# Optimization experiments

Hardware: AMD Instinct MI355X
Metric: run time of the kernel (lower is better)

## Reference

```python
import jax, jax.numpy as jnp
import numpy as np

DIM = 64  # per-head dim; temperature init = sqrt(DIM)
B, H, S, D = 4, 12, 2048, 64


def setup_inputs() -> dict:
    key = jax.random.key(0)
    kq, kk, kv = jax.random.split(key, 3)
    Q = jax.random.normal(kq, (B, H, S, D), dtype=jnp.float32)
    K = jax.random.normal(kk, (B, H, S, D), dtype=jnp.float32)
    V = jax.random.normal(kv, (B, H, S, D), dtype=jnp.float32)
    temperature = jnp.ones((1,), dtype=jnp.float32) * (DIM ** 0.5)
    return {"Q": Q, "K": K, "V": V, "temperature": temperature}


def reference(Q, K, V, temperature):
    # scores: [B,H,S,S]
    scores = jnp.einsum("bhqd,bhkd->bhqk", Q, K) / temperature
    s = scores.shape[-1]
    eye = jnp.eye(s, dtype=bool)  # diagonal self-exclusion
    scores = jnp.where(eye, -jnp.inf, scores)
    attn = jax.nn.softmax(scores, axis=-1)
    return jnp.einsum("bhqk,bhkd->bhqd", attn, V)
```

## Files before the change

### kernel.cpp

```cpp
#include <hip/hip_runtime.h>
#include <hip/hip_bf16.h>

#define S_LEN 2048
#define D_DIM 64
#define NHEADS 48
#define QT 128
#define KT 64
#define NKT (S_LEN / KT)
#define HEAD_ELEMS ((size_t)S_LEN * D_DIM)
#define WS_NEED (3ull * NHEADS * S_LEN * D_DIM * 2ull)

typedef short bf16x8 __attribute__((ext_vector_type(8)));
typedef float f32x4 __attribute__((ext_vector_type(4)));

__device__ __forceinline__ unsigned short f2bf(float x) {
    unsigned u = __builtin_bit_cast(unsigned, x);
    u = (u + 0x7fffu + ((u >> 16) & 1u)) >> 16;
    return (unsigned short)u;
}

__device__ __forceinline__ unsigned cvtpk(float lo, float hi) {
    unsigned r;
    asm("v_cvt_pk_bf16_f32 %0, %1, %2" : "=v"(r) : "v"(lo), "v"(hi));
    return r;
}

__global__ __launch_bounds__(256) void lsa_prep(
    const float* __restrict__ Qg, const float* __restrict__ Kg,
    const float* __restrict__ Vg, const float* __restrict__ Tg,
    unsigned short* __restrict__ Qs, unsigned short* __restrict__ Kf,
    unsigned short* __restrict__ Vf) {
    const int b   = blockIdx.x;
    const int tid = threadIdx.x;
    const int r   = tid >> 4;
    const int c4  = (tid & 15) * 4;

    __shared__ __align__(16) unsigned short Kl[4096];
    __shared__ __align__(16) unsigned short Vl[4096];

    const size_t ibase = (size_t)b * 4096;
    const float qscale = 1.442695041f / Tg[0];

#pragma unroll
    for (int it = 0; it < 4; ++it) {
        const int rr = it * 16 + r;
        const size_t off = ibase + (size_t)rr * D_DIM + c4;

        float4 q4 = *(const float4*)(Qg + off);
        uint2 qo;
        qo.x = cvtpk(q4.x * qscale, q4.y * qscale);
        qo.y = cvtpk(q4.z * qscale, q4.w * qscale);
        *(uint2*)&Qs[off] = qo;

        float4 k4 = *(const float4*)(Kg + off);
        {
            const int f = rr >> 4, l15 = rr & 15;
            const int c = c4 >> 5, lhi = (c4 >> 3) & 3, j0 = c4 & 7;
            uint2 ko;
            ko.x = cvtpk(k4.x, k4.y);
            ko.y = cvtpk(k4.z, k4.w);
            *(uint2*)&Kl[c * 2048 + f * 512 + ((lhi << 4) | l15) * 8 + j0] = ko;
        }

        float4 v4 = *(const float4*)(Vg + off);
        {
            const int cc = rr >> 5, rem = rr & 31;
            const int jv = ((rem >> 4) << 2) | (rem & 3);
            const int lhiv = (rem >> 2) & 3;
            const int g = c4 >> 4;
            const int base = cc * 2048 + g * 512 + (lhiv << 7) + jv;
            Vl[base + ((c4 + 0) & 15) * 8] = f2bf(v4.x);
            Vl[base + ((c4 + 1) & 15) * 8] = f2bf(v4.y);
            Vl[base + ((c4 + 2) & 15) * 8] = f2bf(v4.z);
            Vl[base + ((c4 + 3) & 15) * 8] = f2bf(v4.w);
        }
    }
    __syncthreads();
    const uint4* ks = (const uint4*)Kl;
    const uint4* vs = (const uint4*)Vl;
    uint4* kd = (uint4*)(Kf + ibase);
    uint4* vd = (uint4*)(Vf + ibase);
    kd[tid]       = ks[tid];
    kd[tid + 256] = ks[tid + 256];
    vd[tid]       = vs[tid];
    vd[tid + 256] = vs[tid + 256];
}

__global__ __launch_bounds__(256, 2) void lsa_attn_pipe(
    const unsigned short* __restrict__ Qs, const unsigned short* __restrict__ Kf,
    const unsigned short* __restrict__ Vf, float* __restrict__ Og) {

    const int bid  = blockIdx.x;
    const int xcd  = bid & 7;
    const int idx  = bid >> 3;
    const int bh   = xcd * 6 + (idx >> 4);
    const int qt   = idx & 15;
    const int tid  = threadIdx.x;
    const int wid  = tid >> 6;
    const int lane = tid & 63;
    const int l15  = lane & 15;
    const int lhi  = lane >> 4;

    const unsigned short* Qh = Qs + (size_t)bh * HEAD_ELEMS;
    const char* Kh = (const char*)(Kf + (size_t)bh * HEAD_ELEMS) + lane * 16;
    const char* Vh = (const char*)(Vf + (size_t)bh * HEAD_ELEMS) + lane * 16;
    float* Ob = Og + (size_t)bh * HEAD_ELEMS;

    const int qbase   = qt * QT + wid * 32;
    const int diag_kt = qbase >> 6;

    bf16x8 qf[2][2];
#pragma unroll
    for (int rb = 0; rb < 2; ++rb) {
#pragma unroll
        for (int c = 0; c < 2; ++c) {
            qf[rb][c] = *(const bf16x8*)(Qh + (size_t)(qbase + rb * 16 + l15) * D_DIM
                                            + c * 32 + lhi * 8);
        }
    }

    const f32x4 zero4 = {0.f, 0.f, 0.f, 0.f};
    f32x4 acc[2][4];
    float mrow[2], lp[2];
#pragma unroll
    for (int rb = 0; rb < 2; ++rb) {
#pragma unroll
        for (int g = 0; g < 4; ++g) acc[rb][g] = zero4;
        mrow[rb] = -1e30f; lp[rb] = 0.f;
    }

    bf16x8 kr[8], vr[8];
    f32x4 sf[2][4];
    bf16x8 pb[2][2];

#define LOADK(T) do {                                                          \
    const char* p_ = Kh + (size_t)(T) * 8192;                                  \
    _Pragma("unroll")                                                          \
    for (int u = 0; u < 8; ++u) {                                              \
        kr[u] = *(const bf16x8*)(p_ + (u >> 2) * 4096 + (u & 3) * 1024);       \
    }                                                                          \
} while (0)

#define LOADV(T) do {                                                          \
    const char* p_ = Vh + (size_t)(T) * 8192;                                  \
    _Pragma("unroll")                                                          \
    for (int u = 0; u < 8; ++u) {                                              \
        vr[u] = *(const bf16x8*)(p_ + (u >> 2) * 4096 + (u & 3) * 1024);       \
    }                                                                          \
} while (0)

#define QK() do {                                                              \
    _Pragma("unroll")                                                          \
    for (int rb = 0; rb < 2; ++rb) {                                           \
        _Pragma("unroll")                                                      \
        for (int f = 0; f < 4; ++f) sf[rb][f] = zero4;                         \
    }                                                                          \
    __builtin_amdgcn_s_setprio(1);                                             \
    _Pragma("unroll")                                                          \
    for (int c = 0; c < 2; ++c) {                                              \
        _Pragma("unroll")                                                      \
        for (int rb = 0; rb < 2; ++rb) {                                       \
            _Pragma("unroll")                                                  \
            for (int f = 0; f < 4; ++f) {                                      \
                sf[rb][f] = __builtin_amdgcn_mfma_f32_16x16x32_bf16(           \
                    kr[c * 4 + f], qf[rb][c], sf[rb][f], 0, 0, 0);             \
            }                                                                  \
        }                                                                      \
    }                                                                          \
    __builtin_amdgcn_s_setprio(0);                                             \
} while (0)

#define PV() do {                                                              \
    __builtin_amdgcn_s_setprio(1);                                             \
    _Pragma("unroll")                                                          \
    for (int cc = 0; cc < 2; ++cc) {                                           \
        _Pragma("unroll")                                                      \
        for (int rb = 0; rb < 2; ++rb) {                                       \
            _Pragma("unroll")                                                  \
            for (int g = 0; g < 4; ++g) {                                      \
                acc[rb][g] = __builtin_amdgcn_mfma_f32_16x16x32_bf16(          \
                    vr[cc * 4 + g], pb[rb][cc], acc[rb][g], 0, 0, 0);          \
            }                                                                  \
        }                                                                      \
    }                                                                          \
    __builtin_amdgcn_s_setprio(0);                                             \
} while (0)

#define SM(T) do {                                                             \
    if ((T) == diag_kt) {                                                      \
        const int kb0_ = (T) * KT;                                             \
        _Pragma("unroll")                                                      \
        for (int rb = 0; rb < 2; ++rb) {                                       \
            const int q_ = qbase + rb * 16 + l15;                              \
            _Pragma("unroll")                                                  \
            for (int f = 0; f < 4; ++f) {                                      \
                _Pragma("unroll")                                              \
                for (int i = 0; i < 4; ++i) {                                  \
                    const int k_ = kb0_ + f * 16 + lhi * 4 + i;                \
                    if (q_ == k_) sf[rb][f][i] = -1e30f;                       \
                }                                                              \
            }                                                                  \
        }                                                                      \
    }                                                                          \
    _Pragma("unroll")                                                          \
    for (int rb = 0; rb < 2; ++rb) {                                           \
        f32x4 mv_;                                                             \
        _Pragma("unroll")                                                      \
        for (int i = 0; i < 4; ++i) {                                          \
            mv_[i] = fmaxf(fmaxf(sf[rb][0][i], sf[rb][1][i]),                  \
                           fmaxf(sf[rb][2][i], sf[rb][3][i]));                 \
        }                                                                      \
        const float pm_ = fmaxf(fmaxf(mv_[0], mv_[1]), fmaxf(mv_[2], mv_[3]));  \
        if (__any(pm_ > mrow[rb] + 8.0f)) {                                    \
            float m0_ = pm_;                                                   \
            m0_ = fmaxf(m0_, __shfl_xor(m0_, 16));                             \
            m0_ = fmaxf(m0_, __shfl_xor(m0_, 32));                             \
            const float mnew_ = fmaxf(mrow[rb], m0_);                          \
            const float al_ = __builtin_amdgcn_exp2f(mrow[rb] - mnew_);        \
            mrow[rb] = mnew_;                                                  \
            lp[rb] *= al_;                                                     \
            _Pragma("unroll")                                                  \
            for (int g = 0; g < 4; ++g) acc[rb][g] *= al_;                     \
        }                                                                      \
        f32x4 ps_ = zero4;                                                     \
        _Pragma("unroll")                                                      \
        for (int f = 0; f < 4; ++f) {                                          \
            _Pragma("unroll")                                                  \
            for (int i = 0; i < 4; ++i) {                                      \
                sf[rb][f][i] = __builtin_amdgcn_exp2f(sf[rb][f][i] - mrow[rb]); \
            }                                                                  \
            ps_ += sf[rb][f];                                                  \
        }                                                                      \
        lp[rb] += (ps_[0] + ps_[1]) + (ps_[2] + ps_[3]);                       \
        _Pragma("unroll")                                                      \
        for (int cc = 0; cc < 2; ++cc) {                                       \
            uint4 u_;                                                          \
            u_.x = cvtpk(sf[rb][cc * 2][0],     sf[rb][cc * 2][1]);            \
            u_.y = cvtpk(sf[rb][cc * 2][2],     sf[rb][cc * 2][3]);            \
            u_.z = cvtpk(sf[rb][cc * 2 + 1][0], sf[rb][cc * 2 + 1][1]);        \
            u_.w = cvtpk(sf[rb][cc * 2 + 1][2], sf[rb][cc * 2 + 1][3]);        \
            pb[rb][cc] = __builtin_bit_cast(bf16x8, u_);                       \
        }                                                                      \
    }                                                                          \
} while (0)

    LOADK(0);
    LOADV(0);
    QK();

#pragma unroll 1
    for (int t = 0; t < NKT - 1; ++t) {
        LOADK(t + 1);
        __builtin_amdgcn_sched_barrier(0);
        SM(t);
        QK();
        PV();
        LOADV(t + 1);
    }
    SM(NKT - 1);
    PV();

#undef LOADK
#undef LOADV
#undef QK
#undef PV
#undef SM

#pragma unroll
    for (int rb = 0; rb < 2; ++rb) {
        float l = lp[rb];
        l += __shfl_xor(l, 16);
        l += __shfl_xor(l, 32);
        const float invl = 1.0f / l;
        const int q = qbase + rb * 16 + l15;
#pragma unroll
        for (int g = 0; g < 4; ++g) {
            float4 o;
            o.x = acc[rb][g][0] * invl;
            o.y = acc[rb][g][1] * invl;
            o.z = acc[rb][g][2] * invl;
            o.w = acc[rb][g][3] * invl;
            *(float4*)(Ob + (size_t)q * D_DIM + g * 16 + lhi * 4) = o;
        }
    }
}

__device__ __forceinline__ int swzK_fb(int row, int col) {
    return (row << 6) + (col ^ ((row & 7) << 3));
}
__device__ __forceinline__ int swzV_fb(int row, int col) {
    int f = (row ^ (row >> 3)) & 7;
    return (row << 6) + (col ^ (f << 3));
}

__global__ __launch_bounds__(256, 2) void lsa_attn_fb(
    const float* __restrict__ Qg, const float* __restrict__ Kg,
    const float* __restrict__ Vg, const float* __restrict__ Tg,
    float* __restrict__ Og) {

    const int bid  = blockIdx.x;
    const int bh   = bid >> 4;
    const int qt   = bid & 15;
    const int tid  = threadIdx.x;
    const int wid  = tid >> 6;
    const int lane = tid & 63;
    const int l15  = lane & 15;
    const int lhi  = lane >> 4;

    __shared__ __align__(16) unsigned short Kt[KT * D_DIM];
    __shared__ __align__(16) unsigned short Vt[D_DIM * KT];

    const size_t base = (size_t)bh * HEAD_ELEMS;
    const float* Qb = Qg + base;
    const float* Kb = Kg + base;
    const float* Vb = Vg + base;
    float*       Ob = Og + base;

    const float inv_t = 1.0f / Tg[0];
    const int qbase = qt * QT + wid * 32;
    const int diag_kt = qbase >> 6;

    bf16x8 qf[2][2];
#pragma unroll
    for (int rb = 0; rb < 2; ++rb) {
#pragma unroll
        for (int c = 0; c < 2; ++c) {
            const float* src = Qb + (size_t)(qbase + rb * 16 + l15) * D_DIM + c * 32 + lhi * 8;
            float4 a = *(const float4*)(src);
            float4 b = *(const float4*)(src + 4);
            bf16x8 v;
            v[0] = (short)f2bf(a.x * inv_t); v[1] = (short)f2bf(a.y * inv_t);
            v[2] = (short)f2bf(a.z * inv_t); v[3] = (short)f2bf(a.w * inv_t);
            v[4] = (short)f2bf(b.x * inv_t); v[5] = (short)f2bf(b.y * inv_t);
            v[6] = (short)f2bf(b.z * inv_t); v[7] = (short)f2bf(b.w * inv_t);
            qf[rb][c] = v;
        }
    }

    const f32x4 zero4 = {0.f, 0.f, 0.f, 0.f};
    f32x4 acc[2][4];
    float mrow[2], lrow[2];
#pragma unroll
    for (int rb = 0; rb < 2; ++rb) {
#pragma unroll
        for (int g = 0; g < 4; ++g) acc[rb][g] = zero4;
        mrow[rb] = -1e30f; lrow[rb] = 0.f;
    }

    const int ld_r = tid >> 4;
    const int ld_c = (tid & 15) * 4;
    float4 kreg[4], vreg[4];

#define LOAD_TILE(KT_IDX) do {                                                 \
    const int kb0_ = (KT_IDX) * KT;                                            \
    _Pragma("unroll")                                                          \
    for (int it = 0; it < 4; ++it) {                                           \
        const int r_ = it * 16 + ld_r;                                         \
        kreg[it] = *(const float4*)(Kb + (size_t)(kb0_ + r_) * D_DIM + ld_c);  \
        vreg[it] = *(const float4*)(Vb + (size_t)(kb0_ + r_) * D_DIM + ld_c);  \
    }                                                                          \
} while (0)

    LOAD_TILE(0);

    for (int kt = 0; kt < NKT; ++kt) {
        const int kb0 = kt * KT;
        __syncthreads();
#pragma unroll
        for (int it = 0; it < 4; ++it) {
            const int r = it * 16 + ld_r;
            unsigned lo = (unsigned)f2bf(kreg[it].x) | ((unsigned)f2bf(kreg[it].y) << 16);
            unsigned hi = (unsigned)f2bf(kreg[it].z) | ((unsigned)f2bf(kreg[it].w) << 16);
            *(uint2*)&Kt[swzK_fb(r, ld_c)] = make_uint2(lo, hi);
            Vt[swzV_fb(ld_c + 0, r)] = f2bf(vreg[it].x);
            Vt[swzV_fb(ld_c + 1, r)] = f2bf(vreg[it].y);
            Vt[swzV_fb(ld_c + 2, r)] = f2bf(vreg[it].z);
            Vt[swzV_fb(ld_c + 3, r)] = f2bf(vreg[it].w);
        }
        __syncthreads();
        if (kt + 1 < NKT) LOAD_TILE(kt + 1);

        f32x4 sf[2][4];
#pragma unroll
        for (int rb = 0; rb < 2; ++rb) {
#pragma unroll
            for (int f = 0; f < 4; ++f) sf[rb][f] = zero4;
        }

#pragma unroll
        for (int c = 0; c < 2; ++c) {
            bf16x8 kb[4];
#pragma unroll
            for (int f = 0; f < 4; ++f)
                kb[f] = *(const bf16x8*)&Kt[swzK_fb(f * 16 + l15, c * 32 + lhi * 8)];
#pragma unroll
            for (int rb = 0; rb < 2; ++rb) {
#pragma unroll
                for (int f = 0; f < 4; ++f)
                    sf[rb][f] = __builtin_amdgcn_mfma_f32_16x16x32_bf16(
                        kb[f], qf[rb][c], sf[rb][f], 0, 0, 0);
            }
        }

        if (kt == diag_kt) {
#pragma unroll
            for (int rb = 0; rb < 2; ++rb) {
                const int q = qbase + rb * 16 + l15;
#pragma unroll
                for (int f = 0; f < 4; ++f) {
#pragma unroll
                    for (int i = 0; i < 4; ++i) {
                        const int k = kb0 + f * 16 + lhi * 4 + i;
                        if (q == k) sf[rb][f][i] = -1e30f;
                    }
                }
            }
        }

        bf16x8 pb[2][2];
#pragma unroll
        for (int rb = 0; rb < 2; ++rb) {
            f32x4 mv;
#pragma unroll
            for (int i = 0; i < 4; ++i)
                mv[i] = fmaxf(fmaxf(sf[rb][0][i], sf[rb][1][i]),
                              fmaxf(sf[rb][2][i], sf[rb][3][i]));
            float m0 = fmaxf(fmaxf(mv[0], mv[1]), fmaxf(mv[2], mv[3]));
            m0 = fmaxf(m0, __shfl_xor(m0, 16));
            m0 = fmaxf(m0, __shfl_xor(m0, 32));
            const float mnew  = fmaxf(mrow[rb], m0);
            const float alpha = __expf(mrow[rb] - mnew);
            mrow[rb] = mnew;
            f32x4 ps = zero4;
#pragma unroll
            for (int f = 0; f < 4; ++f) {
#pragma unroll
                for (int i = 0; i < 4; ++i)
                    sf[rb][f][i] = __expf(sf[rb][f][i] - mnew);
                ps += sf[rb][f];
            }
            float s0 = (ps[0] + ps[1]) + (ps[2] + ps[3]);
            s0 += __shfl_xor(s0, 16);
            s0 += __shfl_xor(s0, 32);
            lrow[rb] = lrow[rb] * alpha + s0;
#pragma unroll
            for (int g = 0; g < 4; ++g) acc[rb][g] *= alpha;
#pragma unroll
            for (int cc = 0; cc < 2; ++cc) {
                bf16x8 v;
#pragma unroll
                for (int j = 0; j < 8; ++j)
                    v[j] = (short)f2bf(sf[rb][cc * 2 + (j >> 2)][j & 3]);
                pb[rb][cc] = v;
            }
        }

#pragma unroll
        for (int cc = 0; cc < 2; ++cc) {
            bf16x8 va[4];
#pragma unroll
            for (int g = 0; g < 4; ++g) {
                const int row = g * 16 + l15;
                uint2 lo = *(const uint2*)&Vt[swzV_fb(row, cc * 32 + lhi * 4)];
                uint2 hi = *(const uint2*)&Vt[swzV_fb(row, cc * 32 + 16 + lhi * 4)];
                bf16x8 t;
                ((uint2*)&t)[0] = lo;
                ((uint2*)&t)[1] = hi;
                va[g] = t;
            }
#pragma unroll
            for (int rb = 0; rb < 2; ++rb) {
#pragma unroll
                for (int g = 0; g < 4; ++g)
                    acc[rb][g] = __builtin_amdgcn_mfma_f32_16x16x32_bf16(
                        va[g], pb[rb][cc], acc[rb][g], 0, 0, 0);
            }
        }
    }
#undef LOAD_TILE

#pragma unroll
    for (int rb = 0; rb < 2; ++rb) {
        const float invl = 1.0f / lrow[rb];
        const int q = qbase + rb * 16 + l15;
#pragma unroll
        for (int g = 0; g < 4; ++g) {
            float4 o;
            o.x = acc[rb][g][0] * invl;
            o.y = acc[rb][g][1] * invl;
            o.z = acc[rb][g][2] * invl;
            o.w = acc[rb][g][3] * invl;
            *(float4*)(Ob + (size_t)q * D_DIM + g * 16 + lhi * 4) = o;
        }
    }
}

extern "C" void kernel_launch(void* const* d_in, const int* in_sizes, int n_in,
                              void* d_out, int out_size, void* d_ws, size_t ws_size,
                              hipStream_t stream) {
    const float* Q = (const float*)d_in[0];
    const float* K = (const float*)d_in[1];
    const float* V = (const float*)d_in[2];
    const float* T = (const float*)d_in[3];
    float* O = (float*)d_out;

    if (ws_size >= WS_NEED) {
        unsigned short* Qs = (unsigned short*)d_ws;
        unsigned short* Kf = Qs + NHEADS * HEAD_ELEMS;
        unsigned short* Vf = Kf + NHEADS * HEAD_ELEMS;
        hipLaunchKernelGGL(lsa_prep, dim3(NHEADS * NKT), dim3(256), 0, stream,
                           Q, K, V, T, Qs, Kf, Vf);
        hipLaunchKernelGGL(lsa_attn_pipe, dim3(NHEADS * (S_LEN / QT)), dim3(256), 0, stream,
                           Qs, Kf, Vf, O);
    } else {
        hipLaunchKernelGGL(lsa_attn_fb, dim3(NHEADS * (S_LEN / QT)), dim3(256), 0, stream,
                           Q, K, V, T, O);
    }
}
```

Before: 88.41 us.

## Halve key tile and double-buffer score fragments in attention pipeline

```diff
diff --git a/kernel.cpp b/kernel.cpp
--- a/kernel.cpp
+++ b/kernel.cpp
@@ -5,7 +5,7 @@
 #define D_DIM 64
 #define NHEADS 48
 #define QT 128
-#define KT 64
+#define KT 32
 #define NKT (S_LEN / KT)
 #define HEAD_ELEMS ((size_t)S_LEN * D_DIM)
 #define WS_NEED (3ull * NHEADS * S_LEN * D_DIM * 2ull)
@@ -54,12 +54,13 @@
 
         float4 k4 = *(const float4*)(Kg + off);
         {
-            const int f = rr >> 4, l15 = rr & 15;
+            const int l15 = rr & 15;
             const int c = c4 >> 5, lhi = (c4 >> 3) & 3, j0 = c4 & 7;
             uint2 ko;
             ko.x = cvtpk(k4.x, k4.y);
             ko.y = cvtpk(k4.z, k4.w);
-            *(uint2*)&Kl[c * 2048 + f * 512 + ((lhi << 4) | l15) * 8 + j0] = ko;
+            *(uint2*)&Kl[(rr >> 5) * 2048 + c * 1024 + ((rr >> 4) & 1) * 512
+                         + ((lhi << 4) | l15) * 8 + j0] = ko;
         }
 
         float4 v4 = *(const float4*)(Vg + off);
@@ -86,7 +87,7 @@
     vd[tid + 256] = vs[tid + 256];
 }
 
-__global__ __launch_bounds__(256, 2) void lsa_attn_pipe(
+__global__ __launch_bounds__(256, 3) void lsa_attn_p2(
     const unsigned short* __restrict__ Qs, const unsigned short* __restrict__ Kf,
     const unsigned short* __restrict__ Vf, float* __restrict__ Og) {
 
@@ -107,7 +108,7 @@
     float* Ob = Og + (size_t)bh * HEAD_ELEMS;
 
     const int qbase   = qt * QT + wid * 32;
-    const int diag_kt = qbase >> 6;
+    const int diag_kt = qbase >> 5;
 
     bf16x8 qf[2][2];
 #pragma unroll
@@ -129,31 +130,30 @@
         mrow[rb] = -1e30f; lp[rb] = 0.f;
     }
 
-    bf16x8 kr[8], vr[8];
-    f32x4 sf[2][4];
-    bf16x8 pb[2][2];
+    bf16x8 kr[4], vr[4], pb[2];
+    f32x4 sfA[2][2], sfB[2][2];
 
 #define LOADK(T) do {                                                          \
-    const char* p_ = Kh + (size_t)(T) * 8192;                                  \
-    _Pragma("unroll")                                                          \
-    for (int u = 0; u < 8; ++u) {                                              \
-        kr[u] = *(const bf16x8*)(p_ + (u >> 2) * 4096 + (u & 3) * 1024);       \
+    const char* p_ = Kh + (size_t)(T) * 4096;                                  \
+    _Pragma("unroll")                                                          \
+    for (int u = 0; u < 4; ++u) {                                              \
+        kr[u] = *(const bf16x8*)(p_ + (u >> 1) * 2048 + (u & 1) * 1024);       \
     }                                                                          \
 } while (0)
 
 #define LOADV(T) do {                                                          \
-    const char* p_ = Vh + (size_t)(T) * 8192;                                  \
-    _Pragma("unroll")                                                          \
-    for (int u = 0; u < 8; ++u) {                                              \
-        vr[u] = *(const bf16x8*)(p_ + (u >> 2) * 4096 + (u & 3) * 1024);       \
+    const char* p_ = Vh + (size_t)(T) * 4096;                                  \
+    _Pragma("unroll")                                                          \
+    for (int g = 0; g < 4; ++g) {                                              \
+        vr[g] = *(const bf16x8*)(p_ + g * 1024);                               \
     }                                                                          \
 } while (0)
 
-#define QK() do {                                                              \
+#define QK(SF) do {                                                            \
     _Pragma("unroll")                                                          \
     for (int rb = 0; rb < 2; ++rb) {                                           \
         _Pragma("unroll")                                                      \
-        for (int f = 0; f < 4; ++f) sf[rb][f] = zero4;                         \
+        for (int f = 0; f < 2; ++f) SF[rb][f] = zero4;                         \
     }                                                                          \
     __builtin_amdgcn_s_setprio(1);                                             \
     _Pragma("unroll")                                                          \
@@ -161,9 +161,9 @@
         _Pragma("unroll")                                                      \
         for (int rb = 0; rb < 2; ++rb) {                                       \
             _Pragma("unroll")                                                  \
-            for (int f = 0; f < 4; ++f) {                                      \
-                sf[rb][f] = __builtin_amdgcn_mfma_f32_16x16x32_bf16(           \
-                    kr[c * 4 + f], qf[rb][c], sf[rb][f], 0, 0, 0);             \
+            for (int f = 0; f < 2; ++f) {                                      \
+                SF[rb][f] = __builtin_amdgcn_mfma_f32_16x16x32_bf16(           \
+                    kr[c * 2 + f], qf[rb][c], SF[rb][f], 0, 0, 0);             \
             }                                                                  \
         }                                                                      \
     }                                                                          \
@@ -173,44 +173,38 @@
 #define PV() do {                                                              \
     __builtin_amdgcn_s_setprio(1);                                             \
     _Pragma("unroll")                                                          \
-    for (int cc = 0; cc < 2; ++cc) {                                           \
+    for (int rb = 0; rb < 2; ++rb) {                                           \
         _Pragma("unroll")                                                      \
-        for (int rb = 0; rb < 2; ++rb) {                                       \
-            _Pragma("unroll")                                                  \
-            for (int g = 0; g < 4; ++g) {                                      \
-                acc[rb][g] = __builtin_amdgcn_mfma_f32_16x16x32_bf16(          \
-                    vr[cc * 4 + g], pb[rb][cc], acc[rb][g], 0, 0, 0);          \
-            }                                                                  \
+        for (int g = 0; g < 4; ++g) {                                          \
+            acc[rb][g] = __builtin_amdgcn_mfma_f32_16x16x32_bf16(              \
+                vr[g], pb[rb], acc[rb][g], 0, 0, 0);                           \
         }                                                                      \
     }                                                                          \
     __builtin_amdgcn_s_setprio(0);                                             \
 } while (0)
 
-#define SM(T) do {                                                             \
+#define SMX(T, SF) do {                                                        \
     if ((T) == diag_kt) {                                                      \
-        const int kb0_ = (T) * KT;                                             \
         _Pragma("unroll")                                                      \
         for (int rb = 0; rb < 2; ++rb) {                                       \
             const int q_ = qbase + rb * 16 + l15;                              \
             _Pragma("unroll")                                                  \
-            for (int f = 0; f < 4; ++f) {                                      \
+            for (int f = 0; f < 2; ++f) {                                      \
                 _Pragma("unroll")                                              \
                 for (int i = 0; i < 4; ++i) {                                  \
-                    const int k_ = kb0_ + f * 16 + lhi * 4 + i;                \
-                    if (q_ == k_) sf[rb][f][i] = -1e30f;                       \
+                    const int k_ = (T) * KT + f * 16 + lhi * 4 + i;            \
+                    if (q_ == k_) SF[rb][f][i] = -1e30f;                       \
                 }                                                              \
             }                                                                  \
         }                                                                      \
     }                                                                          \
     _Pragma("unroll")                                                          \
     for (int rb = 0; rb < 2; ++rb) {                                           \
-        f32x4 mv_;                                                             \
-        _Pragma("unroll")                                                      \
-        for (int i = 0; i < 4; ++i) {                                          \
-            mv_[i] = fmaxf(fmaxf(sf[rb][0][i], sf[rb][1][i]),                  \
-                           fmaxf(sf[rb][2][i], sf[rb][3][i]));                 \
-        }                                                                      \
-        const float pm_ = fmaxf(fmaxf(mv_[0], mv_[1]), fmaxf(mv_[2], mv_[3]));  \
+        const float pm_ = fmaxf(                                               \
+            fmaxf(fmaxf(SF[rb][0][0], SF[rb][0][1]),                           \
+                  fmaxf(SF[rb][0][2], SF[rb][0][3])),                          \
+            fmaxf(fmaxf(SF[rb][1][0], SF[rb][1][1]),                           \
+                  fmaxf(SF[rb][1][2], SF[rb][1][3])));                         \
         if (__any(pm_ > mrow[rb] + 8.0f)) {                                    \
             float m0_ = pm_;                                                   \
             m0_ = fmaxf(m0_, __shfl_xor(m0_, 16));                             \
@@ -224,47 +218,53 @@
         }                                                                      \
         f32x4 ps_ = zero4;                                                     \
         _Pragma("unroll")                                                      \
-        for (int f = 0; f < 4; ++f) {                                          \
+        for (int f = 0; f < 2; ++f) {                                          \
             _Pragma("unroll")                                                  \
             for (int i = 0; i < 4; ++i) {                                      \
-                sf[rb][f][i] = __builtin_amdgcn_exp2f(sf[rb][f][i] - mrow[rb]); \
+                SF[rb][f][i] = __builtin_amdgcn_exp2f(SF[rb][f][i] - mrow[rb]); \
             }                                                                  \
-            ps_ += sf[rb][f];                                                  \
+            ps_ += SF[rb][f];                                                  \
         }                                                                      \
         lp[rb] += (ps_[0] + ps_[1]) + (ps_[2] + ps_[3]);                       \
-        _Pragma("unroll")                                                      \
-        for (int cc = 0; cc < 2; ++cc) {                                       \
-            uint4 u_;                                                          \
-            u_.x = cvtpk(sf[rb][cc * 2][0],     sf[rb][cc * 2][1]);            \
-            u_.y = cvtpk(sf[rb][cc * 2][2],     sf[rb][cc * 2][3]);            \
-            u_.z = cvtpk(sf[rb][cc * 2 + 1][0], sf[rb][cc * 2 + 1][1]);        \
-            u_.w = cvtpk(sf[rb][cc * 2 + 1][2], sf[rb][cc * 2 + 1][3]);        \
-            pb[rb][cc] = __builtin_bit_cast(bf16x8, u_);                       \
-        }                                                                      \
+        uint4 u_;                                                              \
+        u_.x = cvtpk(SF[rb][0][0], SF[rb][0][1]);                              \
+        u_.y = cvtpk(SF[rb][0][2], SF[rb][0][3]);                              \
+        u_.z = cvtpk(SF[rb][1][0], SF[rb][1][1]);                              \
+        u_.w = cvtpk(SF[rb][1][2], SF[rb][1][3]);                              \
+        pb[rb] = __builtin_bit_cast(bf16x8, u_);                               \
     }                                                                          \
 } while (0)
 
     LOADK(0);
+    QK(sfA);
+    LOADK(1);
     LOADV(0);
-    QK();
 
 #pragma unroll 1
-    for (int t = 0; t < NKT - 1; ++t) {
-        LOADK(t + 1);
-        __builtin_amdgcn_sched_barrier(0);
-        SM(t);
-        QK();
+    for (int t = 0; t < NKT - 2; t += 2) {
+        QK(sfB);
+        LOADK(t + 2);
+        SMX(t, sfA);
         PV();
         LOADV(t + 1);
-    }
-    SM(NKT - 1);
+        QK(sfA);
+        LOADK(t + 3);
+        SMX(t + 1, sfB);
+        PV();
+        LOADV(t + 2);
+    }
+    QK(sfB);
+    SMX(NKT - 2, sfA);
+    PV();
+    LOADV(NKT - 1);
+    SMX(NKT - 1, sfB);
     PV();
 
 #undef LOADK
 #undef LOADV
 #undef QK
 #undef PV
-#undef SM
+#undef SMX
 
 #pragma unroll
     for (int rb = 0; rb < 2; ++rb) {
@@ -307,8 +307,8 @@
     const int l15  = lane & 15;
     const int lhi  = lane >> 4;
 
-    __shared__ __align__(16) unsigned short Kt[KT * D_DIM];
-    __shared__ __align__(16) unsigned short Vt[D_DIM * KT];
+    __shared__ __align__(16) unsigned short Kt[64 * D_DIM];
+    __shared__ __align__(16) unsigned short Vt[D_DIM * 64];
 
     const size_t base = (size_t)bh * HEAD_ELEMS;
     const float* Qb = Qg + base;
@@ -352,7 +352,7 @@
     float4 kreg[4], vreg[4];
 
 #define LOAD_TILE(KT_IDX) do {                                                 \
-    const int kb0_ = (KT_IDX) * KT;                                            \
+    const int kb0_ = (KT_IDX) * 64;                                            \
     _Pragma("unroll")                                                          \
     for (int it = 0; it < 4; ++it) {                                           \
         const int r_ = it * 16 + ld_r;                                         \
@@ -363,8 +363,8 @@
 
     LOAD_TILE(0);
 
-    for (int kt = 0; kt < NKT; ++kt) {
-        const int kb0 = kt * KT;
+    for (int kt = 0; kt < 32; ++kt) {
+        const int kb0 = kt * 64;
         __syncthreads();
 #pragma unroll
         for (int it = 0; it < 4; ++it) {
@@ -378,7 +378,7 @@
             Vt[swzV_fb(ld_c + 3, r)] = f2bf(vreg[it].w);
         }
         __syncthreads();
-        if (kt + 1 < NKT) LOAD_TILE(kt + 1);
+        if (kt + 1 < 32) LOAD_TILE(kt + 1);
 
         f32x4 sf[2][4];
 #pragma unroll
@@ -508,9 +508,9 @@
         unsigned short* Qs = (unsigned short*)d_ws;
         unsigned short* Kf = Qs + NHEADS * HEAD_ELEMS;
         unsigned short* Vf = Kf + NHEADS * HEAD_ELEMS;
-        hipLaunchKernelGGL(lsa_prep, dim3(NHEADS * NKT), dim3(256), 0, stream,
+        hipLaunchKernelGGL(lsa_prep, dim3(NHEADS * 32), dim3(256), 0, stream,
                            Q, K, V, T, Qs, Kf, Vf);
-        hipLaunchKernelGGL(lsa_attn_pipe, dim3(NHEADS * (S_LEN / QT)), dim3(256), 0, stream,
+        hipLaunchKernelGGL(lsa_attn_p2, dim3(NHEADS * (S_LEN / QT)), dim3(256), 0, stream,
                            Qs, Kf, Vf, O);
     } else {
         hipLaunchKernelGGL(lsa_attn_fb, dim3(NHEADS * (S_LEN / QT)), dim3(256), 0, stream,
```

Result: slower. 91.90 us (+4.0%).

## Use lazy softmax rescaling after first tile and seed QK MFMA with zero

Applied to the files above, without the earlier changes.

```diff
diff --git a/kernel.cpp b/kernel.cpp
--- a/kernel.cpp
+++ b/kernel.cpp
@@ -86,7 +86,7 @@
     vd[tid + 256] = vs[tid + 256];
 }
 
-__global__ __launch_bounds__(256, 2) void lsa_attn_pipe(
+__global__ __launch_bounds__(256, 2) void lsa_attn_p4(
     const unsigned short* __restrict__ Qs, const unsigned short* __restrict__ Kf,
     const unsigned short* __restrict__ Vf, float* __restrict__ Og) {
 
@@ -102,8 +102,8 @@
     const int lhi  = lane >> 4;
 
     const unsigned short* Qh = Qs + (size_t)bh * HEAD_ELEMS;
-    const char* Kh = (const char*)(Kf + (size_t)bh * HEAD_ELEMS) + lane * 16;
-    const char* Vh = (const char*)(Vf + (size_t)bh * HEAD_ELEMS) + lane * 16;
+    const char* kp = (const char*)(Kf + (size_t)bh * HEAD_ELEMS) + lane * 16;
+    const char* vp = (const char*)(Vf + (size_t)bh * HEAD_ELEMS) + lane * 16;
     float* Ob = Og + (size_t)bh * HEAD_ELEMS;
 
     const int qbase   = qt * QT + wid * 32;
@@ -128,43 +128,44 @@
         for (int g = 0; g < 4; ++g) acc[rb][g] = zero4;
         mrow[rb] = -1e30f; lp[rb] = 0.f;
     }
+    const f32x4 zq = zero4;
 
     bf16x8 kr[8], vr[8];
     f32x4 sf[2][4];
     bf16x8 pb[2][2];
 
-#define LOADK(T) do {                                                          \
-    const char* p_ = Kh + (size_t)(T) * 8192;                                  \
+#define LOADK() do {                                                           \
     _Pragma("unroll")                                                          \
     for (int u = 0; u < 8; ++u) {                                              \
-        kr[u] = *(const bf16x8*)(p_ + (u >> 2) * 4096 + (u & 3) * 1024);       \
-    }                                                                          \
-} while (0)
-
-#define LOADV(T) do {                                                          \
-    const char* p_ = Vh + (size_t)(T) * 8192;                                  \
+        kr[u] = *(const bf16x8*)(kp + (u >> 2) * 4096 + (u & 3) * 1024);       \
+    }                                                                          \
+    kp += 8192;                                                                \
+} while (0)
+
+#define LOADV() do {                                                           \
     _Pragma("unroll")                                                          \
     for (int u = 0; u < 8; ++u) {                                              \
-        vr[u] = *(const bf16x8*)(p_ + (u >> 2) * 4096 + (u & 3) * 1024);       \
-    }                                                                          \
+        vr[u] = *(const bf16x8*)(vp + (u >> 2) * 4096 + (u & 3) * 1024);       \
+    }                                                                          \
+    vp += 8192;                                                                \
 } while (0)
 
 #define QK() do {                                                              \
+    __builtin_amdgcn_s_setprio(1);                                             \
     _Pragma("unroll")                                                          \
     for (int rb = 0; rb < 2; ++rb) {                                           \
         _Pragma("unroll")                                                      \
-        for (int f = 0; f < 4; ++f) sf[rb][f] = zero4;                         \
-    }                                                                          \
-    __builtin_amdgcn_s_setprio(1);                                             \
-    _Pragma("unroll")                                                          \
-    for (int c = 0; c < 2; ++c) {                                              \
-        _Pragma("unroll")                                                      \
-        for (int rb = 0; rb < 2; ++rb) {                                       \
-            _Pragma("unroll")                                                  \
-            for (int f = 0; f < 4; ++f) {                                      \
-                sf[rb][f] = __builtin_amdgcn_mfma_f32_16x16x32_bf16(           \
-                    kr[c * 4 + f], qf[rb][c], sf[rb][f], 0, 0, 0);             \
-            }                                                                  \
+        for (int f = 0; f < 4; ++f) {                                          \
+            sf[rb][f] = __builtin_amdgcn_mfma_f32_16x16x32_bf16(               \
+                kr[f], qf[rb][0], zq, 0, 0, 0);                                \
+        }                                                                      \
+    }                                                                          \
+    _Pragma("unroll")                                                          \
+    for (int rb = 0; rb < 2; ++rb) {                                           \
+        _Pragma("unroll")                                                      \
+        for (int f = 0; f < 4; ++f) {                                          \
+            sf[rb][f] = __builtin_amdgcn_mfma_f32_16x16x32_bf16(               \
+                kr[4 + f], qf[rb][1], sf[rb][f], 0, 0, 0);                     \
         }                                                                      \
     }                                                                          \
     __builtin_amdgcn_s_setprio(0);                                             \
@@ -186,9 +187,8 @@
     __builtin_amdgcn_s_setprio(0);                                             \
 } while (0)
 
-#define SM(T) do {                                                             \
+#define DIAG(T) do {                                                           \
     if ((T) == diag_kt) {                                                      \
-        const int kb0_ = (T) * KT;                                             \
         _Pragma("unroll")                                                      \
         for (int rb = 0; rb < 2; ++rb) {                                       \
             const int q_ = qbase + rb * 16 + l15;                              \
@@ -196,12 +196,28 @@
             for (int f = 0; f < 4; ++f) {                                      \
                 _Pragma("unroll")                                              \
                 for (int i = 0; i < 4; ++i) {                                  \
-                    const int k_ = kb0_ + f * 16 + lhi * 4 + i;                \
+                    const int k_ = (T) * KT + f * 16 + lhi * 4 + i;            \
                     if (q_ == k_) sf[rb][f][i] = -1e30f;                       \
                 }                                                              \
             }                                                                  \
         }                                                                      \
     }                                                                          \
+} while (0)
+
+#define PACK(rb) do {                                                          \
+    _Pragma("unroll")                                                          \
+    for (int cc = 0; cc < 2; ++cc) {                                           \
+        uint4 u_;                                                              \
+        u_.x = cvtpk(sf[rb][cc * 2][0],     sf[rb][cc * 2][1]);                \
+        u_.y = cvtpk(sf[rb][cc * 2][2],     sf[rb][cc * 2][3]);                \
+        u_.z = cvtpk(sf[rb][cc * 2 + 1][0], sf[rb][cc * 2 + 1][1]);            \
+        u_.w = cvtpk(sf[rb][cc * 2 + 1][2], sf[rb][cc * 2 + 1][3]);            \
+        pb[rb][cc] = __builtin_bit_cast(bf16x8, u_);                           \
+    }                                                                          \
+} while (0)
+
+#define SM_FULL(T) do {                                                        \
+    DIAG(T);                                                                   \
     _Pragma("unroll")                                                          \
     for (int rb = 0; rb < 2; ++rb) {                                           \
         f32x4 mv_;                                                             \
@@ -232,39 +248,77 @@
             ps_ += sf[rb][f];                                                  \
         }                                                                      \
         lp[rb] += (ps_[0] + ps_[1]) + (ps_[2] + ps_[3]);                       \
-        _Pragma("unroll")                                                      \
-        for (int cc = 0; cc < 2; ++cc) {                                       \
-            uint4 u_;                                                          \
-            u_.x = cvtpk(sf[rb][cc * 2][0],     sf[rb][cc * 2][1]);            \
-            u_.y = cvtpk(sf[rb][cc * 2][2],     sf[rb][cc * 2][3]);            \
-            u_.z = cvtpk(sf[rb][cc * 2 + 1][0], sf[rb][cc * 2 + 1][1]);        \
-            u_.w = cvtpk(sf[rb][cc * 2 + 1][2], sf[rb][cc * 2 + 1][3]);        \
-            pb[rb][cc] = __builtin_bit_cast(bf16x8, u_);                       \
-        }                                                                      \
-    }                                                                          \
-} while (0)
-
-    LOADK(0);
-    LOADV(0);
+        PACK(rb);                                                              \
+    }                                                                          \
+} while (0)
+
+#define SM_FAST(T) do {                                                        \
+    DIAG(T);                                                                   \
+    _Pragma("unroll")                                                          \
+    for (int rb = 0; rb < 2; ++rb) {                                           \
+        f32x4 ps_ = zero4;                                                     \
+        _Pragma("unroll")                                                      \
+        for (int f = 0; f < 4; ++f) {                                          \
+            _Pragma("unroll")                                                  \
+            for (int i = 0; i < 4; ++i) {                                      \
+                sf[rb][f][i] = __builtin_amdgcn_exp2f(sf[rb][f][i] - mrow[rb]); \
+            }                                                                  \
+            ps_ += sf[rb][f];                                                  \
+        }                                                                      \
+        const float s0_ = (ps_[0] + ps_[1]) + (ps_[2] + ps_[3]);               \
+        if (__any(s0_ > 256.0f)) {                                             \
+            f32x4 mv_;                                                         \
+            _Pragma("unroll")                                                  \
+            for (int i = 0; i < 4; ++i) {                                      \
+                mv_[i] = fmaxf(fmaxf(sf[rb][0][i], sf[rb][1][i]),              \
+                               fmaxf(sf[rb][2][i], sf[rb][3][i]));             \
+            }                                                                  \
+            float mx_ = fmaxf(fmaxf(mv_[0], mv_[1]), fmaxf(mv_[2], mv_[3]));    \
+            mx_ = fmaxf(mx_, __shfl_xor(mx_, 16));                             \
+            mx_ = fmaxf(mx_, __shfl_xor(mx_, 32));                             \
+            mx_ = fmaxf(mx_, 1.0f);                                            \
+            const float L_  = __log2f(mx_);                                    \
+            const float al_ = __builtin_amdgcn_exp2f(-L_);                     \
+            mrow[rb] += L_;                                                    \
+            _Pragma("unroll")                                                  \
+            for (int f = 0; f < 4; ++f) {                                      \
+                _Pragma("unroll")                                              \
+                for (int i = 0; i < 4; ++i) sf[rb][f][i] *= al_;               \
+            }                                                                  \
+            _Pragma("unroll")                                                  \
+            for (int g = 0; g < 4; ++g) acc[rb][g] *= al_;                     \
+            lp[rb] = (lp[rb] + s0_) * al_;                                     \
+        } else {                                                               \
+            lp[rb] += s0_;                                                     \
+        }                                                                      \
+        PACK(rb);                                                              \
+    }                                                                          \
+} while (0)
+
+    LOADK();
+    LOADV();
     QK();
 
 #pragma unroll 1
     for (int t = 0; t < NKT - 1; ++t) {
-        LOADK(t + 1);
+        LOADK();
         __builtin_amdgcn_sched_barrier(0);
-        SM(t);
+        if (t == 0) { SM_FULL(0); } else { SM_FAST(t); }
         QK();
         PV();
-        LOADV(t + 1);
-    }
-    SM(NKT - 1);
+        LOADV();
+    }
+    SM_FAST(NKT - 1);
     PV();
 
 #undef LOADK
 #undef LOADV
 #undef QK
 #undef PV
-#undef SM
+#undef DIAG
+#undef PACK
+#undef SM_FULL
+#undef SM_FAST
 
 #pragma unroll
     for (int rb = 0; rb < 2; ++rb) {
@@ -307,8 +361,8 @@
     const int l15  = lane & 15;
     const int lhi  = lane >> 4;
 
-    __shared__ __align__(16) unsigned short Kt[KT * D_DIM];
-    __shared__ __align__(16) unsigned short Vt[D_DIM * KT];
+    __shared__ __align__(16) unsigned short Kt[64 * D_DIM];
+    __shared__ __align__(16) unsigned short Vt[D_DIM * 64];
 
     const size_t base = (size_t)bh * HEAD_ELEMS;
     const float* Qb = Qg + base;
@@ -352,7 +406,7 @@
     float4 kreg[4], vreg[4];
 
 #define LOAD_TILE(KT_IDX) do {                                                 \
-    const int kb0_ = (KT_IDX) * KT;                                            \
+    const int kb0_ = (KT_IDX) * 64;                                            \
     _Pragma("unroll")                                                          \
     for (int it = 0; it < 4; ++it) {                                           \
         const int r_ = it * 16 + ld_r;                                         \
@@ -363,8 +417,8 @@
 
     LOAD_TILE(0);
 
-    for (int kt = 0; kt < NKT; ++kt) {
-        const int kb0 = kt * KT;
+    for (int kt = 0; kt < 32; ++kt) {
+        const int kb0 = kt * 64;
         __syncthreads();
 #pragma unroll
         for (int it = 0; it < 4; ++it) {
@@ -378,7 +432,7 @@
             Vt[swzV_fb(ld_c + 3, r)] = f2bf(vreg[it].w);
         }
         __syncthreads();
-        if (kt + 1 < NKT) LOAD_TILE(kt + 1);
+        if (kt + 1 < 32) LOAD_TILE(kt + 1);
 
         f32x4 sf[2][4];
 #pragma unroll
@@ -510,7 +564,7 @@
         unsigned short* Vf = Kf + NHEADS * HEAD_ELEMS;
         hipLaunchKernelGGL(lsa_prep, dim3(NHEADS * NKT), dim3(256), 0, stream,
                            Q, K, V, T, Qs, Kf, Vf);
-        hipLaunchKernelGGL(lsa_attn_pipe, dim3(NHEADS * (S_LEN / QT)), dim3(256), 0, stream,
+        hipLaunchKernelGGL(lsa_attn_p4, dim3(NHEADS * (S_LEN / QT)), dim3(256), 0, stream,
                            Qs, Kf, Vf, O);
     } else {
         hipLaunchKernelGGL(lsa_attn_fb, dim3(NHEADS * (S_LEN / QT)), dim3(256), 0, stream,
```

Measured after the change: 93.07 us. +5.3%, slower.

## Stage K/V tiles through double-buffered LDS via direct global-to-LDS loads

Applied to the files above, without the earlier changes.

```diff
diff --git a/kernel.cpp b/kernel.cpp
--- a/kernel.cpp
+++ b/kernel.cpp
@@ -23,6 +23,12 @@
     unsigned r;
     asm("v_cvt_pk_bf16_f32 %0, %1, %2" : "=v"(r) : "v"(lo), "v"(hi));
     return r;
+}
+
+__device__ __forceinline__ void gload16(const void* g, void* l) {
+    __builtin_amdgcn_global_load_lds(
+        (const __attribute__((address_space(1))) unsigned int*)g,
+        (__attribute__((address_space(3))) unsigned int*)l, 16, 0, 0);
 }
 
 __global__ __launch_bounds__(256) void lsa_prep(
@@ -86,7 +92,7 @@
     vd[tid + 256] = vs[tid + 256];
 }
 
-__global__ __launch_bounds__(256, 2) void lsa_attn_pipe(
+__global__ __launch_bounds__(256, 2) void lsa_attn_lds(
     const unsigned short* __restrict__ Qs, const unsigned short* __restrict__ Kf,
     const unsigned short* __restrict__ Vf, float* __restrict__ Og) {
 
@@ -101,9 +107,11 @@
     const int l15  = lane & 15;
     const int lhi  = lane >> 4;
 
+    __shared__ __align__(16) unsigned short KV[2][2][KT * D_DIM];
+
     const unsigned short* Qh = Qs + (size_t)bh * HEAD_ELEMS;
-    const char* Kh = (const char*)(Kf + (size_t)bh * HEAD_ELEMS) + lane * 16;
-    const char* Vh = (const char*)(Vf + (size_t)bh * HEAD_ELEMS) + lane * 16;
+    const char* Kh = (const char*)(Kf + (size_t)bh * HEAD_ELEMS);
+    const char* Vh = (const char*)(Vf + (size_t)bh * HEAD_ELEMS);
     float* Ob = Og + (size_t)bh * HEAD_ELEMS;
 
     const int qbase   = qt * QT + wid * 32;
@@ -129,45 +137,54 @@
         mrow[rb] = -1e30f; lp[rb] = 0.f;
     }
 
-    bf16x8 kr[8], vr[8];
+    bf16x8 vr[8];
     f32x4 sf[2][4];
     bf16x8 pb[2][2];
 
-#define LOADK(T) do {                                                          \
-    const char* p_ = Kh + (size_t)(T) * 8192;                                  \
-    _Pragma("unroll")                                                          \
-    for (int u = 0; u < 8; ++u) {                                              \
-        kr[u] = *(const bf16x8*)(p_ + (u >> 2) * 4096 + (u & 3) * 1024);       \
-    }                                                                          \
+#define ISSUE(BUF, T) do {                                                     \
+    const char* ks_ = Kh + (size_t)(T) * 8192 + wid * 2048;                    \
+    const char* vs_ = Vh + (size_t)(T) * 8192 + wid * 2048;                    \
+    char* lk_ = (char*)&KV[BUF][0][0] + wid * 2048;                            \
+    char* lv_ = (char*)&KV[BUF][1][0] + wid * 2048;                            \
+    gload16(ks_ + lane * 16, lk_);                                             \
+    gload16(ks_ + 1024 + lane * 16, lk_ + 1024);                               \
+    gload16(vs_ + lane * 16, lv_);                                             \
+    gload16(vs_ + 1024 + lane * 16, lv_ + 1024);                               \
 } while (0)
 
-#define LOADV(T) do {                                                          \
-    const char* p_ = Vh + (size_t)(T) * 8192;                                  \
-    _Pragma("unroll")                                                          \
-    for (int u = 0; u < 8; ++u) {                                              \
-        vr[u] = *(const bf16x8*)(p_ + (u >> 2) * 4096 + (u & 3) * 1024);       \
-    }                                                                          \
-} while (0)
-
-#define QK() do {                                                              \
+#define DSQK(BUF) do {                                                         \
+    const char* lk_ = (const char*)&KV[BUF][0][0] + lane * 16;                 \
     _Pragma("unroll")                                                          \
     for (int rb = 0; rb < 2; ++rb) {                                           \
         _Pragma("unroll")                                                      \
         for (int f = 0; f < 4; ++f) sf[rb][f] = zero4;                         \
     }                                                                          \
-    __builtin_amdgcn_s_setprio(1);                                             \
     _Pragma("unroll")                                                          \
     for (int c = 0; c < 2; ++c) {                                              \
+        bf16x8 kb_[4];                                                         \
+        _Pragma("unroll")                                                      \
+        for (int f = 0; f < 4; ++f) {                                          \
+            kb_[f] = *(const bf16x8*)(lk_ + c * 4096 + f * 1024);              \
+        }                                                                      \
+        __builtin_amdgcn_s_setprio(1);                                         \
         _Pragma("unroll")                                                      \
         for (int rb = 0; rb < 2; ++rb) {                                       \
             _Pragma("unroll")                                                  \
             for (int f = 0; f < 4; ++f) {                                      \
                 sf[rb][f] = __builtin_amdgcn_mfma_f32_16x16x32_bf16(           \
-                    kr[c * 4 + f], qf[rb][c], sf[rb][f], 0, 0, 0);             \
+                    kb_[f], qf[rb][c], sf[rb][f], 0, 0, 0);                    \
             }                                                                  \
         }                                                                      \
-    }                                                                          \
-    __builtin_amdgcn_s_setprio(0);                                             \
+        __builtin_amdgcn_s_setprio(0);                                         \
+    }                                                                          \
+} while (0)
+
+#define DSV(BUF) do {                                                          \
+    const char* lv_ = (const char*)&KV[BUF][1][0] + lane * 16;                 \
+    _Pragma("unroll")                                                          \
+    for (int u = 0; u < 8; ++u) {                                              \
+        vr[u] = *(const bf16x8*)(lv_ + (u >> 2) * 4096 + (u & 3) * 1024);      \
+    }                                                                          \
 } while (0)
 
 #define PV() do {                                                              \
@@ -186,9 +203,8 @@
     __builtin_amdgcn_s_setprio(0);                                             \
 } while (0)
 
-#define SM(T) do {                                                             \
+#define SMX(T) do {                                                            \
     if ((T) == diag_kt) {                                                      \
-        const int kb0_ = (T) * KT;                                             \
         _Pragma("unroll")                                                      \
         for (int rb = 0; rb < 2; ++rb) {                                       \
             const int q_ = qbase + rb * 16 + l15;                              \
@@ -196,7 +212,7 @@
             for (int f = 0; f < 4; ++f) {                                      \
                 _Pragma("unroll")                                              \
                 for (int i = 0; i < 4; ++i) {                                  \
-                    const int k_ = kb0_ + f * 16 + lhi * 4 + i;                \
+                    const int k_ = (T) * KT + f * 16 + lhi * 4 + i;            \
                     if (q_ == k_) sf[rb][f][i] = -1e30f;                       \
                 }                                                              \
             }                                                                  \
@@ -244,27 +260,29 @@
     }                                                                          \
 } while (0)
 
-    LOADK(0);
-    LOADV(0);
-    QK();
+    ISSUE(0, 0);
+    __syncthreads();
+    ISSUE(1, 1);
+    DSQK(0);
+    DSV(0);
 
 #pragma unroll 1
     for (int t = 0; t < NKT - 1; ++t) {
-        LOADK(t + 1);
-        __builtin_amdgcn_sched_barrier(0);
-        SM(t);
-        QK();
+        SMX(t);
         PV();
-        LOADV(t + 1);
-    }
-    SM(NKT - 1);
+        __syncthreads();
+        if (t + 2 < NKT) ISSUE(t & 1, t + 2);
+        DSQK((t + 1) & 1);
+        DSV((t + 1) & 1);
+    }
+    SMX(NKT - 1);
     PV();
 
-#undef LOADK
-#undef LOADV
-#undef QK
+#undef ISSUE
+#undef DSQK
+#undef DSV
 #undef PV
-#undef SM
+#undef SMX
 
 #pragma unroll
     for (int rb = 0; rb < 2; ++rb) {
@@ -307,8 +325,8 @@
     const int l15  = lane & 15;
     const int lhi  = lane >> 4;
 
-    __shared__ __align__(16) unsigned short Kt[KT * D_DIM];
-    __shared__ __align__(16) unsigned short Vt[D_DIM * KT];
+    __shared__ __align__(16) unsigned short Kt[64 * D_DIM];
+    __shared__ __align__(16) unsigned short Vt[D_DIM * 64];
 
     const size_t base = (size_t)bh * HEAD_ELEMS;
     const float* Qb = Qg + base;
@@ -352,7 +370,7 @@
     float4 kreg[4], vreg[4];
 
 #define LOAD_TILE(KT_IDX) do {                                                 \
-    const int kb0_ = (KT_IDX) * KT;                                            \
+    const int kb0_ = (KT_IDX) * 64;                                            \
     _Pragma("unroll")                                                          \
     for (int it = 0; it < 4; ++it) {                                           \
         const int r_ = it * 16 + ld_r;                                         \
@@ -363,8 +381,8 @@
 
     LOAD_TILE(0);
 
-    for (int kt = 0; kt < NKT; ++kt) {
-        const int kb0 = kt * KT;
+    for (int kt = 0; kt < 32; ++kt) {
+        const int kb0 = kt * 64;
         __syncthreads();
 #pragma unroll
         for (int it = 0; it < 4; ++it) {
@@ -378,7 +396,7 @@
             Vt[swzV_fb(ld_c + 3, r)] = f2bf(vreg[it].w);
         }
         __syncthreads();
-        if (kt + 1 < NKT) LOAD_TILE(kt + 1);
+        if (kt + 1 < 32) LOAD_TILE(kt + 1);
 
         f32x4 sf[2][4];
 #pragma unroll
@@ -510,7 +528,7 @@
         unsigned short* Vf = Kf + NHEADS * HEAD_ELEMS;
         hipLaunchKernelGGL(lsa_prep, dim3(NHEADS * NKT), dim3(256), 0, stream,
                            Q, K, V, T, Qs, Kf, Vf);
-        hipLaunchKernelGGL(lsa_attn_pipe, dim3(NHEADS * (S_LEN / QT)), dim3(256), 0, stream,
+        hipLaunchKernelGGL(lsa_attn_lds, dim3(NHEADS * (S_LEN / QT)), dim3(256), 0, stream,
                            Qs, Kf, Vf, O);
     } else {
         hipLaunchKernelGGL(lsa_attn_fb, dim3(NHEADS * (S_LEN / QT)), dim3(256), 0, stream,
```

Measured after the change: 87.74 us (median of 2 runs). Within noise of the previous version (-0.8%).
